# Performance work log

Measured on AMD Instinct MI355X. Metric: run time of the kernel, lower is better.

Reference implementation:

```python
import jax, jax.numpy as jnp
import numpy as np

B, Q, K, D = 32, 1024, 1024, 128

def setup_inputs() -> dict:
    key = jax.random.key(0)
    kq, kk, kv, kl = jax.random.split(key, 4)
    return {
        "queries": jax.random.normal(kq, (B, Q, D), dtype=jnp.float32),
        "keys": jax.random.normal(kk, (B, K, D), dtype=jnp.float32),
        "values": jax.random.normal(kv, (B, K, D), dtype=jnp.float32),
        "valid_length": jax.random.randint(kl, (B,), 1, K + 1),
    }

def reference(queries, keys, values, valid_length):
    d = queries.shape[-1]
    # scores: [B, Q, K]
    scores = jnp.einsum("bqd,bkd->bqk", queries, keys) / jnp.sqrt(jnp.float32(d))
    # length mask: position k is valid iff k < valid_length[b]
    mask = jnp.arange(keys.shape[1])[None, None, :] < valid_length[:, None, None]
    scores = jnp.where(mask, scores, jnp.float32(-1e9))
    attn = jax.nn.softmax(scores, axis=-1)
    # dropout module is identity in eval / p=0
    return jnp.einsum("bqk,bkv->bqv", attn, values)
```

## Files before the change

### kernel.cpp

```cpp
#include <hip/hip_runtime.h>
#include <hip/hip_bf16.h>
#include <stdint.h>

#define B_    32
#define QLEN  1024
#define KSEQ  1024
#define DIM   128
#define NKT   (KSEQ / 64)
#define SCALE 0.08838834764831845f

typedef __attribute__((ext_vector_type(8))) short  short8;
typedef __attribute__((ext_vector_type(4))) float  floatx4;
typedef unsigned int u32;

__device__ __forceinline__ u32 f2bf(float x) {
  union { float f; u32 u; } v; v.f = x;
  return (v.u + 0x7FFF + ((v.u >> 16) & 1)) >> 16;
}
__device__ __forceinline__ u32 pack2(float lo, float hi) {
  return f2bf(lo) | (f2bf(hi) << 16);
}

__device__ __forceinline__ void barrier_full() {
  asm volatile("s_waitcnt vmcnt(0) lgkmcnt(0)" ::: "memory");
  __syncthreads();
}

__global__ __launch_bounds__(256) void prep_kernel(const float* __restrict__ Kg,
                                                   const float* __restrict__ Vg,
                                                   uint4* __restrict__ Ksw,
                                                   uint4* __restrict__ Vsw) {
  const int kt = blockIdx.x, b = blockIdx.y, t = threadIdx.x;
  if (blockIdx.z == 0) {
    const float* src = Kg + ((size_t)b * KSEQ + kt * 64) * DIM;
    uint4* dst = Ksw + ((size_t)b * NKT + kt) * 1024;
#pragma unroll
    for (int it = 0; it < 4; it++) {
      const int f = it * 256 + t, r = f >> 4, c = f & 15;
      floatx4 f0 = *(const floatx4*)(src + r * DIM + c * 8);
      floatx4 f1 = *(const floatx4*)(src + r * DIM + c * 8 + 4);
      uint4 o;
      o.x = pack2(f0[0], f0[1]); o.y = pack2(f0[2], f0[3]);
      o.z = pack2(f1[0], f1[1]); o.w = pack2(f1[2], f1[3]);
      dst[r * 16 + (c ^ (r & 15))] = o;
    }
  } else {
    __shared__ float Vt[64][132];
    const float* src = Vg + ((size_t)b * KSEQ + kt * 64) * DIM;
#pragma unroll
    for (int it = 0; it < 8; it++) {
      const int f = it * 256 + t, r = f >> 5, c4 = (f & 31) * 4;
      *(floatx4*)&Vt[r][c4] = *(const floatx4*)(src + r * DIM + c4);
    }
    __syncthreads();
    uint4* dst = Vsw + ((size_t)b * NKT + kt) * 1024;
#pragma unroll
    for (int it = 0; it < 4; it++) {
      const int g = it * 256 + t, d = g >> 3, kc = g & 7;
      uint4 o;
      o.x = pack2(Vt[kc * 8 + 0][d], Vt[kc * 8 + 1][d]);
      o.y = pack2(Vt[kc * 8 + 2][d], Vt[kc * 8 + 3][d]);
      o.z = pack2(Vt[kc * 8 + 4][d], Vt[kc * 8 + 5][d]);
      o.w = pack2(Vt[kc * 8 + 6][d], Vt[kc * 8 + 7][d]);
      dst[d * 8 + (kc ^ (d & 7))] = o;
    }
  }
}

typedef const __attribute__((address_space(1))) u32* as1p;
typedef __attribute__((address_space(3))) u32* as3p;
__device__ __forceinline__ void gl_lds16(const void* g, void* l) {
  __builtin_amdgcn_global_load_lds((as1p)g, (as3p)l, 16, 0, 0);
}

__global__ __launch_bounds__(256, 2) void attn_kernel(
    const float* __restrict__ Qg, const uint4* __restrict__ Ksw,
    const uint4* __restrict__ Vsw, const int* __restrict__ vlen,
    float* __restrict__ Og) {
  __shared__ __align__(16) short Kbuf[64 * 128];
  __shared__ __align__(16) short Vbuf[2][128 * 64];
  __shared__ __align__(16) short Pl[4][16][72];

  const int b = blockIdx.y, q0 = blockIdx.x * 64;
  const int t = threadIdx.x, wave = t >> 6, lane = t & 63;
  const int quad = lane >> 4, m = lane & 15;
  const int L  = vlen[b];
  const int nt = (L + 63) >> 6;

  const char* Kt = (const char*)(Ksw + (size_t)b * NKT * 1024);
  const char* Vt = (const char*)(Vsw + (size_t)b * NKT * 1024);

  short8 aq[4];
  {
    const float* qrow = Qg + ((size_t)b * QLEN + q0 + wave * 16 + m) * DIM;
#pragma unroll
    for (int c = 0; c < 4; c++) {
      floatx4 f0 = *(const floatx4*)(qrow + c * 32 + quad * 8);
      floatx4 f1 = *(const floatx4*)(qrow + c * 32 + quad * 8 + 4);
      short8 a;
      a[0] = (short)f2bf(f0[0]); a[1] = (short)f2bf(f0[1]);
      a[2] = (short)f2bf(f0[2]); a[3] = (short)f2bf(f0[3]);
      a[4] = (short)f2bf(f1[0]); a[5] = (short)f2bf(f1[1]);
      a[6] = (short)f2bf(f1[2]); a[7] = (short)f2bf(f1[3]);
      aq[c] = a;
    }
  }

  float mrow[4], lrow[4];
  floatx4 oacc[8];
#pragma unroll
  for (int r = 0; r < 4; r++) { mrow[r] = -INFINITY; lrow[r] = 0.0f; }
#pragma unroll
  for (int d = 0; d < 8; d++) oacc[d] = (floatx4){0.f, 0.f, 0.f, 0.f};

#define ISSUE_K(tk)                                                          \
  {                                                                          \
    const char* g_ = Kt + (size_t)(tk) * 16384 + wave * 4096 + lane * 16;    \
    _Pragma("unroll") for (int i_ = 0; i_ < 4; i_++)                         \
        gl_lds16(g_ + i_ * 1024, (char*)Kbuf + wave * 4096 + i_ * 1024);     \
  }
#define ISSUE_V(tk, bb)                                                      \
  {                                                                          \
    const char* g_ = Vt + (size_t)(tk) * 16384 + wave * 4096 + lane * 16;    \
    _Pragma("unroll") for (int i_ = 0; i_ < 4; i_++)                         \
        gl_lds16(g_ + i_ * 1024, (char*)Vbuf[bb] + wave * 4096 + i_ * 1024); \
  }

  ISSUE_K(0);
  ISSUE_V(0, 0);

  for (int tk = 0; tk < nt; tk++) {
    const int k0 = tk * 64;
    barrier_full();

    floatx4 sa[4];
#pragma unroll
    for (int s = 0; s < 4; s++) sa[s] = (floatx4){0.f, 0.f, 0.f, 0.f};
#pragma unroll
    for (int s = 0; s < 4; s++) {
#pragma unroll
      for (int c = 0; c < 4; c++) {
        const short8 bk = *(const short8*)(Kbuf + (s * 16 + m) * 128 +
                                           (((c * 4 + quad) ^ m) & 15) * 8);
        sa[s] = __builtin_amdgcn_mfma_f32_16x16x32_bf16(aq[c], bk, sa[s], 0, 0, 0);
      }
    }

    float p[4][4], mx[4];
    const bool vv0 = (k0 + m) < L,      vv1 = (k0 + 16 + m) < L;
    const bool vv2 = (k0 + 32 + m) < L, vv3 = (k0 + 48 + m) < L;
#pragma unroll
    for (int r = 0; r < 4; r++) {
      p[0][r] = vv0 ? sa[0][r] * SCALE : -INFINITY;
      p[1][r] = vv1 ? sa[1][r] * SCALE : -INFINITY;
      p[2][r] = vv2 ? sa[2][r] * SCALE : -INFINITY;
      p[3][r] = vv3 ? sa[3][r] * SCALE : -INFINITY;
      mx[r] = fmaxf(fmaxf(p[0][r], p[1][r]), fmaxf(p[2][r], p[3][r]));
    }
#pragma unroll
    for (int off = 1; off < 16; off <<= 1) {
#pragma unroll
      for (int r = 0; r < 4; r++) mx[r] = fmaxf(mx[r], __shfl_xor(mx[r], off));
    }
    float al[4], ts[4];
#pragma unroll
    for (int r = 0; r < 4; r++) {
      const float mn = fmaxf(mrow[r], mx[r]);
      al[r] = __expf(mrow[r] - mn);
      mrow[r] = mn;
#pragma unroll
      for (int s = 0; s < 4; s++) p[s][r] = __expf(p[s][r] - mn);
      ts[r] = (p[0][r] + p[1][r]) + (p[2][r] + p[3][r]);
    }
#pragma unroll
    for (int off = 1; off < 16; off <<= 1) {
#pragma unroll
      for (int r = 0; r < 4; r++) ts[r] += __shfl_xor(ts[r], off);
    }
#pragma unroll
    for (int r = 0; r < 4; r++) lrow[r] = lrow[r] * al[r] + ts[r];
#pragma unroll
    for (int d = 0; d < 8; d++) {
#pragma unroll
      for (int r = 0; r < 4; r++) oacc[d][r] *= al[r];
    }

#pragma unroll
    for (int s = 0; s < 4; s++) {
#pragma unroll
      for (int r = 0; r < 4; r++)
        Pl[wave][quad * 4 + r][s * 16 + m] = (short)f2bf(p[s][r]);
    }
    asm volatile("s_waitcnt lgkmcnt(0)" ::: "memory");
    const short8 pa0 = *(const short8*)&Pl[wave][m][quad * 8];
    const short8 pa1 = *(const short8*)&Pl[wave][m][32 + quad * 8];

    barrier_full();
    if (tk + 1 < nt) {
      ISSUE_K(tk + 1);
      ISSUE_V(tk + 1, (tk + 1) & 1);
    }

    const short* Vb_ = Vbuf[tk & 1];
#pragma unroll
    for (int d = 0; d < 8; d++) {
      const int row = d * 16 + m;
      const short8 bv0 = *(const short8*)(Vb_ + row * 64 + ((quad ^ (m & 7)) & 7) * 8);
      const short8 bv1 = *(const short8*)(Vb_ + row * 64 + (((quad + 4) ^ (m & 7)) & 7) * 8);
      oacc[d] = __builtin_amdgcn_mfma_f32_16x16x32_bf16(pa0, bv0, oacc[d], 0, 0, 0);
      oacc[d] = __builtin_amdgcn_mfma_f32_16x16x32_bf16(pa1, bv1, oacc[d], 0, 0, 0);
    }
  }

  float inv[4];
#pragma unroll
  for (int r = 0; r < 4; r++) inv[r] = 1.0f / lrow[r];
  float* orow = Og + ((size_t)b * QLEN + q0 + wave * 16) * DIM;
#pragma unroll
  for (int d = 0; d < 8; d++) {
#pragma unroll
    for (int r = 0; r < 4; r++)
      orow[(size_t)(quad * 4 + r) * DIM + d * 16 + m] = oacc[d][r] * inv[r];
  }
#undef ISSUE_K
#undef ISSUE_V
}

extern "C" void kernel_launch(void* const* d_in, const int* in_sizes, int n_in,
                              void* d_out, int out_size, void* d_ws, size_t ws_size,
                              hipStream_t stream) {
  const float* Qg = (const float*)d_in[0];
  const float* Kg = (const float*)d_in[1];
  const float* Vg = (const float*)d_in[2];
  const int*  vln = (const int*)d_in[3];
  uint4* Ksw = (uint4*)d_ws;
  uint4* Vsw = (uint4*)((char*)d_ws + (size_t)B_ * NKT * 16384);

  prep_kernel<<<dim3(NKT, B_, 2), 256, 0, stream>>>(Kg, Vg, Ksw, Vsw);
  attn_kernel<<<dim3(QLEN / 64, B_), 256, 0, stream>>>(Qg, Ksw, Vsw, vln,
                                                       (float*)d_out);
}
```

Baseline: 132.0 us.

## Rewrite attention kernel with 32x32 MFMA, 128-query tiles and double-buffered K/V

Replaces the 16x16 MFMA flash-attention kernel with one using 32x32x16 bf16 MFMAs. Each block now covers 128 queries, so K/V are reused over twice as many rows, and both K and V are double-buffered with a single barrier per tile. Q is staged through LDS, the computed S^T layout lets each lane hold one query's softmax state so reductions need only one cross-half shuffle, and rescaling is skipped when the max does not change. The prep kernel skips key tiles past valid_length and loads V transposed straight from global without LDS. In exchange, occupancy drops to one block per CU, the grid is half as large, and register pressure rises.

```diff
diff --git a/kernel.cpp b/kernel.cpp
--- a/kernel.cpp
+++ b/kernel.cpp
@@ -8,9 +8,11 @@
 #define DIM   128
 #define NKT   (KSEQ / 64)
 #define SCALE 0.08838834764831845f
-
-typedef __attribute__((ext_vector_type(8))) short  short8;
-typedef __attribute__((ext_vector_type(4))) float  floatx4;
+#define NEGBIG (-1e30f)
+
+typedef __attribute__((ext_vector_type(8)))  short  short8;
+typedef __attribute__((ext_vector_type(4)))  float  floatx4;
+typedef __attribute__((ext_vector_type(16))) float  floatx16;
 typedef unsigned int u32;
 
 __device__ __forceinline__ u32 f2bf(float x) {
@@ -25,12 +27,17 @@
   asm volatile("s_waitcnt vmcnt(0) lgkmcnt(0)" ::: "memory");
   __syncthreads();
 }
+__device__ __forceinline__ void barrier_lgkm() {
+  asm volatile("s_waitcnt lgkmcnt(0)\ns_barrier" ::: "memory");
+}
 
 __global__ __launch_bounds__(256) void prep_kernel(const float* __restrict__ Kg,
                                                    const float* __restrict__ Vg,
+                                                   const int* __restrict__ vlen,
                                                    uint4* __restrict__ Ksw,
                                                    uint4* __restrict__ Vsw) {
   const int kt = blockIdx.x, b = blockIdx.y, t = threadIdx.x;
+  if (kt * 64 >= vlen[b]) return;
   if (blockIdx.z == 0) {
     const float* src = Kg + ((size_t)b * KSEQ + kt * 64) * DIM;
     uint4* dst = Ksw + ((size_t)b * NKT + kt) * 1024;
@@ -45,23 +52,17 @@
       dst[r * 16 + (c ^ (r & 15))] = o;
     }
   } else {
-    __shared__ float Vt[64][132];
     const float* src = Vg + ((size_t)b * KSEQ + kt * 64) * DIM;
-#pragma unroll
-    for (int it = 0; it < 8; it++) {
-      const int f = it * 256 + t, r = f >> 5, c4 = (f & 31) * 4;
-      *(floatx4*)&Vt[r][c4] = *(const floatx4*)(src + r * DIM + c4);
-    }
-    __syncthreads();
     uint4* dst = Vsw + ((size_t)b * NKT + kt) * 1024;
 #pragma unroll
     for (int it = 0; it < 4; it++) {
-      const int g = it * 256 + t, d = g >> 3, kc = g & 7;
+      const int id = it * 256 + t, d = id & 127, kc = id >> 7;
+      float v[8];
+#pragma unroll
+      for (int j = 0; j < 8; j++) v[j] = src[(size_t)(kc * 8 + j) * DIM + d];
       uint4 o;
-      o.x = pack2(Vt[kc * 8 + 0][d], Vt[kc * 8 + 1][d]);
-      o.y = pack2(Vt[kc * 8 + 2][d], Vt[kc * 8 + 3][d]);
-      o.z = pack2(Vt[kc * 8 + 4][d], Vt[kc * 8 + 5][d]);
-      o.w = pack2(Vt[kc * 8 + 6][d], Vt[kc * 8 + 7][d]);
+      o.x = pack2(v[0], v[1]); o.y = pack2(v[2], v[3]);
+      o.z = pack2(v[4], v[5]); o.w = pack2(v[6], v[7]);
       dst[d * 8 + (kc ^ (d & 7))] = o;
     }
   }
@@ -73,154 +74,167 @@
   __builtin_amdgcn_global_load_lds((as1p)g, (as3p)l, 16, 0, 0);
 }
 
-__global__ __launch_bounds__(256, 2) void attn_kernel(
+__global__ __launch_bounds__(256, 1) void attn_kernel(
     const float* __restrict__ Qg, const uint4* __restrict__ Ksw,
     const uint4* __restrict__ Vsw, const int* __restrict__ vlen,
     float* __restrict__ Og) {
-  __shared__ __align__(16) short Kbuf[64 * 128];
-  __shared__ __align__(16) short Vbuf[2][128 * 64];
-  __shared__ __align__(16) short Pl[4][16][72];
-
-  const int b = blockIdx.y, q0 = blockIdx.x * 64;
+  __shared__ __align__(16) char pool[82432];
+
+  const int b = blockIdx.y, q0 = blockIdx.x * 128;
   const int t = threadIdx.x, wave = t >> 6, lane = t & 63;
-  const int quad = lane >> 4, m = lane & 15;
-  const int L  = vlen[b];
-  const int nt = (L + 63) >> 6;
+  const int l31 = lane & 31, h = lane >> 5;
+  const int L = vlen[b], nt = (L + 63) >> 6;
 
   const char* Kt = (const char*)(Ksw + (size_t)b * NKT * 1024);
   const char* Vt = (const char*)(Vsw + (size_t)b * NKT * 1024);
-
-  short8 aq[4];
+  short* Pw = (short*)(pool + 65536) + wave * 2112;
+
   {
-    const float* qrow = Qg + ((size_t)b * QLEN + q0 + wave * 16 + m) * DIM;
-#pragma unroll
-    for (int c = 0; c < 4; c++) {
-      floatx4 f0 = *(const floatx4*)(qrow + c * 32 + quad * 8);
-      floatx4 f1 = *(const floatx4*)(qrow + c * 32 + quad * 8 + 4);
+    const char* g = (const char*)(Qg + ((size_t)b * QLEN + q0) * DIM) +
+                    wave * 16384 + lane * 16;
+    char* l = pool + wave * 16384 + lane * 16;
+#pragma unroll
+    for (int i = 0; i < 16; i++) gl_lds16(g + i * 1024, l + i * 1024);
+  }
+  barrier_full();
+  short8 aq[8];
+  {
+    const float* qrow = (const float*)(pool + wave * 16384) + l31 * 128;
+#pragma unroll
+    for (int s = 0; s < 8; s++) {
+      floatx4 f0 = *(const floatx4*)(qrow + s * 16 + h * 8);
+      floatx4 f1 = *(const floatx4*)(qrow + s * 16 + h * 8 + 4);
       short8 a;
       a[0] = (short)f2bf(f0[0]); a[1] = (short)f2bf(f0[1]);
       a[2] = (short)f2bf(f0[2]); a[3] = (short)f2bf(f0[3]);
       a[4] = (short)f2bf(f1[0]); a[5] = (short)f2bf(f1[1]);
       a[6] = (short)f2bf(f1[2]); a[7] = (short)f2bf(f1[3]);
-      aq[c] = a;
-    }
-  }
-
-  float mrow[4], lrow[4];
-  floatx4 oacc[8];
-#pragma unroll
-  for (int r = 0; r < 4; r++) { mrow[r] = -INFINITY; lrow[r] = 0.0f; }
-#pragma unroll
-  for (int d = 0; d < 8; d++) oacc[d] = (floatx4){0.f, 0.f, 0.f, 0.f};
-
-#define ISSUE_K(tk)                                                          \
-  {                                                                          \
-    const char* g_ = Kt + (size_t)(tk) * 16384 + wave * 4096 + lane * 16;    \
-    _Pragma("unroll") for (int i_ = 0; i_ < 4; i_++)                         \
-        gl_lds16(g_ + i_ * 1024, (char*)Kbuf + wave * 4096 + i_ * 1024);     \
-  }
-#define ISSUE_V(tk, bb)                                                      \
-  {                                                                          \
-    const char* g_ = Vt + (size_t)(tk) * 16384 + wave * 4096 + lane * 16;    \
-    _Pragma("unroll") for (int i_ = 0; i_ < 4; i_++)                         \
-        gl_lds16(g_ + i_ * 1024, (char*)Vbuf[bb] + wave * 4096 + i_ * 1024); \
-  }
-
-  ISSUE_K(0);
+      aq[s] = a;
+    }
+  }
+  barrier_lgkm();
+
+  floatx16 oacc[4];
+#pragma unroll
+  for (int d = 0; d < 4; d++)
+#pragma unroll
+    for (int r = 0; r < 16; r++) oacc[d][r] = 0.f;
+  float mrun = NEGBIG, lrun = 0.f;
+
+#define ISSUE_K(tk, bb)                                                       \
+  {                                                                           \
+    const char* g_ = Kt + (size_t)(tk) * 16384 + wave * 4096 + lane * 16;     \
+    char* l_ = pool + (bb) * 16384 + wave * 4096 + lane * 16;                 \
+    _Pragma("unroll") for (int i_ = 0; i_ < 4; i_++)                          \
+        gl_lds16(g_ + i_ * 1024, l_ + i_ * 1024);                             \
+  }
+#define ISSUE_V(tk, bb)                                                       \
+  {                                                                           \
+    const char* g_ = Vt + (size_t)(tk) * 16384 + wave * 4096 + lane * 16;     \
+    char* l_ = pool + 32768 + (bb) * 16384 + wave * 4096 + lane * 16;         \
+    _Pragma("unroll") for (int i_ = 0; i_ < 4; i_++)                          \
+        gl_lds16(g_ + i_ * 1024, l_ + i_ * 1024);                             \
+  }
+
+  ISSUE_K(0, 0);
   ISSUE_V(0, 0);
 
   for (int tk = 0; tk < nt; tk++) {
-    const int k0 = tk * 64;
     barrier_full();
-
-    floatx4 sa[4];
-#pragma unroll
-    for (int s = 0; s < 4; s++) sa[s] = (floatx4){0.f, 0.f, 0.f, 0.f};
+    if (tk + 1 < nt) { ISSUE_K(tk + 1, (tk + 1) & 1); ISSUE_V(tk + 1, (tk + 1) & 1); }
+    const short* Kb_ = (const short*)(pool + (tk & 1) * 16384);
+    const short* Vb_ = (const short*)(pool + 32768 + (tk & 1) * 16384);
+
+    floatx16 st0, st1;
+#pragma unroll
+    for (int r = 0; r < 16; r++) { st0[r] = 0.f; st1[r] = 0.f; }
+#pragma unroll
+    for (int s = 0; s < 8; s++) {
+      const int pos = (((s * 2 + h) ^ (l31 & 15))) * 8;
+      const short8 k0 = *(const short8*)(Kb_ + l31 * 128 + pos);
+      const short8 k1 = *(const short8*)(Kb_ + (32 + l31) * 128 + pos);
+      st0 = __builtin_amdgcn_mfma_f32_32x32x16_bf16(k0, aq[s], st0, 0, 0, 0);
+      st1 = __builtin_amdgcn_mfma_f32_32x32x16_bf16(k1, aq[s], st1, 0, 0, 0);
+    }
+
+    const int rem = L - tk * 64;
+    float p0[16], p1[16];
+    if (rem >= 64) {
+#pragma unroll
+      for (int r = 0; r < 16; r++) { p0[r] = st0[r] * SCALE; p1[r] = st1[r] * SCALE; }
+    } else {
+#pragma unroll
+      for (int r = 0; r < 16; r++) {
+        const int kl = (r & 3) + 8 * (r >> 2) + 4 * h;
+        p0[r] = (kl < rem)      ? st0[r] * SCALE : NEGBIG;
+        p1[r] = (kl + 32 < rem) ? st1[r] * SCALE : NEGBIG;
+      }
+    }
+
+    float mt = fmaxf(p0[0], p1[0]);
+#pragma unroll
+    for (int r = 1; r < 16; r++) mt = fmaxf(mt, fmaxf(p0[r], p1[r]));
+    mt = fmaxf(mt, __shfl_xor(mt, 32));
+    const float mnew = fmaxf(mrun, mt);
+    const float alpha = __expf(mrun - mnew);
+    const bool need = mnew > mrun;
+    mrun = mnew;
+    float lt = 0.f;
+#pragma unroll
+    for (int r = 0; r < 16; r++) {
+      p0[r] = __expf(p0[r] - mnew);
+      p1[r] = __expf(p1[r] - mnew);
+      lt += p0[r] + p1[r];
+    }
+    lt += __shfl_xor(lt, 32);
+    lrun = lrun * alpha + lt;
+    if (__ballot(need) != 0ull) {
+#pragma unroll
+      for (int r = 0; r < 16; r++) {
+        const float ar = __shfl(alpha, (r & 3) + 8 * (r >> 2) + 4 * h);
+        oacc[0][r] *= ar; oacc[1][r] *= ar; oacc[2][r] *= ar; oacc[3][r] *= ar;
+      }
+    }
+
+#pragma unroll
+    for (int r = 0; r < 16; r++) {
+      const int kl = (r & 3) + 8 * (r >> 2) + 4 * h;
+      Pw[l31 * 66 + kl]      = (short)f2bf(p0[r]);
+      Pw[l31 * 66 + 32 + kl] = (short)f2bf(p1[r]);
+    }
+    asm volatile("s_waitcnt lgkmcnt(0)" ::: "memory");
+    short8 pf[4];
 #pragma unroll
     for (int s = 0; s < 4; s++) {
-#pragma unroll
-      for (int c = 0; c < 4; c++) {
-        const short8 bk = *(const short8*)(Kbuf + (s * 16 + m) * 128 +
-                                           (((c * 4 + quad) ^ m) & 15) * 8);
-        sa[s] = __builtin_amdgcn_mfma_f32_16x16x32_bf16(aq[c], bk, sa[s], 0, 0, 0);
+      const u32* pp = (const u32*)Pw + l31 * 33 + s * 8 + h * 4;
+      short8 f;
+      ((u32*)&f)[0] = pp[0]; ((u32*)&f)[1] = pp[1];
+      ((u32*)&f)[2] = pp[2]; ((u32*)&f)[3] = pp[3];
+      pf[s] = f;
+    }
+
+#pragma unroll
+    for (int ds_ = 0; ds_ < 4; ds_++) {
+      const int d = ds_ * 32 + l31;
+#pragma unroll
+      for (int s = 0; s < 4; s++) {
+        const short8 vf =
+            *(const short8*)(Vb_ + d * 64 + (((s * 2 + h) ^ (d & 7)) * 8));
+        oacc[ds_] = __builtin_amdgcn_mfma_f32_32x32x16_bf16(pf[s], vf, oacc[ds_], 0, 0, 0);
       }
     }
-
-    float p[4][4], mx[4];
-    const bool vv0 = (k0 + m) < L,      vv1 = (k0 + 16 + m) < L;
-    const bool vv2 = (k0 + 32 + m) < L, vv3 = (k0 + 48 + m) < L;
-#pragma unroll
-    for (int r = 0; r < 4; r++) {
-      p[0][r] = vv0 ? sa[0][r] * SCALE : -INFINITY;
-      p[1][r] = vv1 ? sa[1][r] * SCALE : -INFINITY;
-      p[2][r] = vv2 ? sa[2][r] * SCALE : -INFINITY;
-      p[3][r] = vv3 ? sa[3][r] * SCALE : -INFINITY;
-      mx[r] = fmaxf(fmaxf(p[0][r], p[1][r]), fmaxf(p[2][r], p[3][r]));
-    }
-#pragma unroll
-    for (int off = 1; off < 16; off <<= 1) {
-#pragma unroll
-      for (int r = 0; r < 4; r++) mx[r] = fmaxf(mx[r], __shfl_xor(mx[r], off));
-    }
-    float al[4], ts[4];
-#pragma unroll
-    for (int r = 0; r < 4; r++) {
-      const float mn = fmaxf(mrow[r], mx[r]);
-      al[r] = __expf(mrow[r] - mn);
-      mrow[r] = mn;
-#pragma unroll
-      for (int s = 0; s < 4; s++) p[s][r] = __expf(p[s][r] - mn);
-      ts[r] = (p[0][r] + p[1][r]) + (p[2][r] + p[3][r]);
-    }
-#pragma unroll
-    for (int off = 1; off < 16; off <<= 1) {
-#pragma unroll
-      for (int r = 0; r < 4; r++) ts[r] += __shfl_xor(ts[r], off);
-    }
-#pragma unroll
-    for (int r = 0; r < 4; r++) lrow[r] = lrow[r] * al[r] + ts[r];
-#pragma unroll
-    for (int d = 0; d < 8; d++) {
-#pragma unroll
-      for (int r = 0; r < 4; r++) oacc[d][r] *= al[r];
-    }
-
-#pragma unroll
-    for (int s = 0; s < 4; s++) {
-#pragma unroll
-      for (int r = 0; r < 4; r++)
-        Pl[wave][quad * 4 + r][s * 16 + m] = (short)f2bf(p[s][r]);
-    }
-    asm volatile("s_waitcnt lgkmcnt(0)" ::: "memory");
-    const short8 pa0 = *(const short8*)&Pl[wave][m][quad * 8];
-    const short8 pa1 = *(const short8*)&Pl[wave][m][32 + quad * 8];
-
-    barrier_full();
-    if (tk + 1 < nt) {
-      ISSUE_K(tk + 1);
-      ISSUE_V(tk + 1, (tk + 1) & 1);
-    }
-
-    const short* Vb_ = Vbuf[tk & 1];
-#pragma unroll
-    for (int d = 0; d < 8; d++) {
-      const int row = d * 16 + m;
-      const short8 bv0 = *(const short8*)(Vb_ + row * 64 + ((quad ^ (m & 7)) & 7) * 8);
-      const short8 bv1 = *(const short8*)(Vb_ + row * 64 + (((quad + 4) ^ (m & 7)) & 7) * 8);
-      oacc[d] = __builtin_amdgcn_mfma_f32_16x16x32_bf16(pa0, bv0, oacc[d], 0, 0, 0);
-      oacc[d] = __builtin_amdgcn_mfma_f32_16x16x32_bf16(pa1, bv1, oacc[d], 0, 0, 0);
-    }
-  }
-
-  float inv[4];
-#pragma unroll
-  for (int r = 0; r < 4; r++) inv[r] = 1.0f / lrow[r];
-  float* orow = Og + ((size_t)b * QLEN + q0 + wave * 16) * DIM;
-#pragma unroll
-  for (int d = 0; d < 8; d++) {
-#pragma unroll
-    for (int r = 0; r < 4; r++)
-      orow[(size_t)(quad * 4 + r) * DIM + d * 16 + m] = oacc[d][r] * inv[r];
+  }
+
+  float* obase = Og + ((size_t)b * QLEN + q0 + wave * 32) * DIM;
+#pragma unroll
+  for (int r = 0; r < 16; r++) {
+    const int m = (r & 3) + 8 * (r >> 2) + 4 * h;
+    const float inv = 1.0f / __shfl(lrun, m);
+    float* orow = obase + (size_t)m * DIM + l31;
+    orow[0]  = oacc[0][r] * inv;
+    orow[32] = oacc[1][r] * inv;
+    orow[64] = oacc[2][r] * inv;
+    orow[96] = oacc[3][r] * inv;
   }
 #undef ISSUE_K
 #undef ISSUE_V
@@ -236,7 +250,7 @@
   uint4* Ksw = (uint4*)d_ws;
   uint4* Vsw = (uint4*)((char*)d_ws + (size_t)B_ * NKT * 16384);
 
-  prep_kernel<<<dim3(NKT, B_, 2), 256, 0, stream>>>(Kg, Vg, Ksw, Vsw);
-  attn_kernel<<<dim3(QLEN / 64, B_), 256, 0, stream>>>(Qg, Ksw, Vsw, vln,
-                                                       (float*)d_out);
-}
+  prep_kernel<<<dim3(NKT, B_, 2), 256, 0, stream>>>(Kg, Vg, vln, Ksw, Vsw);
+  attn_kernel<<<dim3(QLEN / 128, B_), 256, 0, stream>>>(Qg, Ksw, Vsw, vln,
+                                                        (float*)d_out);
+}
```

Measured after the change: 136.9 us. 1.04x slower.
